# Kernel tuning notes

Hardware: AMD Instinct MI355X
Metric: run time of the kernel (lower is better)

Reference implementation:

```python
import jax, jax.numpy as jnp
import numpy as np
from jax import lax

B, T, D = 8, 2048, 1024
DECAY = 0.99
EPS = 1e-5


def _layer_norm(x, w, b):
    mu = jnp.mean(x, axis=-1, keepdims=True)
    var = jnp.var(x, axis=-1, keepdims=True)
    return (x - mu) * lax.rsqrt(var + EPS) * w + b


def _fixed_decay_scan(v, decay):
    # h_t = decay * h_{t-1} + v_t along axis=1, h_0 = v_0 (zero initial state)
    a = jnp.full_like(v, decay)

    def combine(c1, c2):
        a1, b1 = c1
        a2, b2 = c2
        return (a1 * a2, a2 * b1 + b2)

    _, h = lax.associative_scan(combine, (a, v), axis=1)
    return h


def setup_inputs() -> dict:
    key = jax.random.key(0)
    ks = jax.random.split(key, 12)
    s = 0.02
    return {
        "x": jax.random.normal(ks[0], (B, T, D), dtype=jnp.float32),
        "mask": jnp.ones((B, T), dtype=jnp.float32),
        "ln1_w": jnp.ones((D,), jnp.float32),
        "ln1_b": jnp.zeros((D,), jnp.float32),
        "ln2_w": jnp.ones((D,), jnp.float32),
        "ln2_b": jnp.zeros((D,), jnp.float32),
        "Wg_f": jax.random.normal(ks[1], (D, D), jnp.float32) * s,
        "bg_f": jnp.ones((D,), jnp.float32),
        "Wg_b": jax.random.normal(ks[2], (D, D), jnp.float32) * s,
        "bg_b": jnp.ones((D,), jnp.float32),
        "W_fuse": jax.random.normal(ks[3], (2 * D, D), jnp.float32) * s,
        "b_fuse": jnp.zeros((D,), jnp.float32),
        "W_ffn1": jax.random.normal(ks[4], (D, 2 * D), jnp.float32) * s,
        "b_ffn1": jnp.zeros((2 * D,), jnp.float32),
        "W_ffn2": jax.random.normal(ks[5], (2 * D, D), jnp.float32) * s,
        "b_ffn2": jnp.zeros((D,), jnp.float32),
    }


def reference(x, mask, ln1_w, ln1_b, ln2_w, ln2_b, Wg_f, bg_f, Wg_b, bg_b,
              W_fuse, b_fuse, W_ffn1, b_ffn1, W_ffn2, b_ffn2):
    residual = x
    h = _layer_norm(x, ln1_w, ln1_b)
    m = mask[..., None]  # (B,T,1)

    # forward-direction gated scan
    v_fwd = jax.nn.sigmoid(h @ Wg_f + bg_f) * h * m
    h_fwd = _fixed_decay_scan(v_fwd, DECAY)

    # backward-direction gated scan (scan over reversed time)
    v_bwd = jax.nn.sigmoid(h @ Wg_b + bg_b) * h * m
    h_bwd = jnp.flip(_fixed_decay_scan(jnp.flip(v_bwd, axis=1), DECAY), axis=1)

    # learned fusion gate
    beta = jax.nn.sigmoid(jnp.concatenate([h_fwd, h_bwd], axis=-1) @ W_fuse + b_fuse)
    fused = beta * h_fwd + (1.0 - beta) * h_bwd

    x = residual + fused  # dropout is identity in eval mode

    # FFN block (exact GELU as torch nn.GELU default)
    ffn = jax.nn.gelu(_layer_norm(x, ln2_w, ln2_b) @ W_ffn1 + b_ffn1, approximate=False) @ W_ffn2 + b_ffn2
    return x + ffn
```

## Files before the change

kernel.cpp:

```cpp
#include <hip/hip_runtime.h>
#include <math.h>

#define Bq 8
#define Tq 2048
#define Dq 1024
#define Mq (Bq*Tq)
#define NCHq 32
#define CHUNKq 64
#define DECAYq 0.99f
#define DF64q 0.52559646f
#define SGq (Bq*NCHq*4)
#define CEBNDq ((size_t)Bq*NCHq*Dq)

typedef unsigned short u16;
typedef unsigned int u32;
typedef __attribute__((ext_vector_type(8))) short bf16x8;
typedef __attribute__((ext_vector_type(4))) float f32x4;
typedef __attribute__((ext_vector_type(4))) u16 u16x4;

__device__ __forceinline__ u16 f2bf(float f) {
  u32 u = __builtin_bit_cast(u32, f);
  return (u16)((u + 0x7FFFu + ((u >> 16) & 1u)) >> 16);
}
__device__ __forceinline__ float bf2f(u16 h) {
  return __builtin_bit_cast(float, (u32)h << 16);
}
__device__ __forceinline__ float sigm(float x) { return 1.0f / (1.0f + expf(-x)); }

__global__ __launch_bounds__(256)
void transpose_all(const float* __restrict__ s0, u16* __restrict__ d0,
                   const float* __restrict__ s1, u16* __restrict__ d1,
                   const float* __restrict__ s2, u16* __restrict__ d2,
                   const float* __restrict__ s3, u16* __restrict__ d3,
                   const float* __restrict__ s4, u16* __restrict__ d4) {
  const int bid = blockIdx.x;
  const float* src; u16* dst; int K, N, local;
  if (bid < 1024)      { src = s0; dst = d0; K = 1024; N = 1024; local = bid; }
  else if (bid < 2048) { src = s1; dst = d1; K = 1024; N = 1024; local = bid - 1024; }
  else if (bid < 4096) { src = s2; dst = d2; K = 2048; N = 1024; local = bid - 2048; }
  else if (bid < 6144) { src = s3; dst = d3; K = 1024; N = 2048; local = bid - 4096; }
  else                 { src = s4; dst = d4; K = 2048; N = 1024; local = bid - 6144; }
  const int ntx = N >> 5;
  const int n0 = (local % ntx) << 5;
  const int k0 = (local / ntx) << 5;
  __shared__ float tile[32][33];
  const int tx = threadIdx.x & 31;
  const int ty = threadIdx.x >> 5;
#pragma unroll
  for (int j = 0; j < 32; j += 8)
    tile[ty + j][tx] = src[(size_t)(k0 + ty + j) * N + (n0 + tx)];
  __syncthreads();
#pragma unroll
  for (int j = 0; j < 32; j += 8)
    dst[(size_t)(n0 + ty + j) * K + (k0 + tx)] = f2bf(tile[tx][ty + j]);
}

__global__ __launch_bounds__(256)
void ln_kernel(const float* __restrict__ xin, const float* __restrict__ w,
               const float* __restrict__ bb, u16* __restrict__ obf) {
  const int row = blockIdx.x;
  const int tid = threadIdx.x;
  const float4 v = ((const float4*)(xin + (size_t)row * Dq))[tid];
  float s  = v.x + v.y + v.z + v.w;
  float s2 = v.x*v.x + v.y*v.y + v.z*v.z + v.w*v.w;
#pragma unroll
  for (int o = 32; o > 0; o >>= 1) { s += __shfl_xor(s, o); s2 += __shfl_xor(s2, o); }
  __shared__ float rs[4], rq[4];
  const int wid = tid >> 6;
  if ((tid & 63) == 0) { rs[wid] = s; rq[wid] = s2; }
  __syncthreads();
  s  = rs[0] + rs[1] + rs[2] + rs[3];
  s2 = rq[0] + rq[1] + rq[2] + rq[3];
  const float mu  = s * (1.0f/Dq);
  const float var = s2 * (1.0f/Dq) - mu*mu;
  const float inv = rsqrtf(var + 1e-5f);
  const float4 wv = ((const float4*)w)[tid];
  const float4 bv = ((const float4*)bb)[tid];
  float4 o;
  o.x = (v.x - mu)*inv*wv.x + bv.x;
  o.y = (v.y - mu)*inv*wv.y + bv.y;
  o.z = (v.z - mu)*inv*wv.z + bv.z;
  o.w = (v.w - mu)*inv*wv.w + bv.w;
  u16x4 ob; ob[0] = f2bf(o.x); ob[1] = f2bf(o.y); ob[2] = f2bf(o.z); ob[3] = f2bf(o.w);
  ((u16x4*)(obf + (size_t)row * Dq))[tid] = ob;
}

__global__ __launch_bounds__(256)
void scan_pass1_dual(const u16* __restrict__ vf, const u16* __restrict__ vb,
                     float* __restrict__ ce) {
  int bid = blockIdx.x;
  const bool rev = bid >= SGq;
  if (rev) bid -= SGq;
  const int dblk = bid & 3;
  const int c    = (bid >> 2) & 31;
  const int b    = bid >> 7;
  const int d    = (dblk << 8) + threadIdx.x;
  const u16* v   = rev ? vb : vf;
  float* cep     = ce + (rev ? CEBNDq : 0);
  const long step = rev ? -(long)Dq : (long)Dq;
  size_t idx = ((size_t)b * Tq + (rev ? (Tq - 1 - c * CHUNKq) : c * CHUNKq)) * Dq + d;
  float e = 0.0f;
  for (int i = 0; i < CHUNKq; ++i) { e = DECAYq * e + bf2f(v[idx]); idx += step; }
  cep[((size_t)b * NCHq + c) * Dq + d] = e;
}

__global__ __launch_bounds__(256)
void scan_pass2_dual(const float* __restrict__ ce, float* __restrict__ car) {
  const int idx = blockIdx.x * 256 + threadIdx.x;
  const int dir = idx >> 13;
  const int loc = idx & 8191;
  const int b = loc >> 10;
  const int d = loc & 1023;
  const size_t base = (size_t)dir * CEBNDq;
  float c = 0.0f;
  for (int k = 0; k < NCHq; ++k) {
    const size_t i = base + ((size_t)b * NCHq + k) * Dq + d;
    car[i] = c;
    c = DF64q * c + ce[i];
  }
}

__global__ __launch_bounds__(256)
void scan_pass3_dual(u16* __restrict__ vf, u16* __restrict__ vb,
                     const float* __restrict__ car) {
  int bid = blockIdx.x;
  const bool rev = bid >= SGq;
  if (rev) bid -= SGq;
  const int dblk = bid & 3;
  const int c    = (bid >> 2) & 31;
  const int b    = bid >> 7;
  const int d    = (dblk << 8) + threadIdx.x;
  u16* v = rev ? vb : vf;
  const float* carp = car + (rev ? CEBNDq : 0);
  float hc = carp[((size_t)b * NCHq + c) * Dq + d];
  const long step = rev ? -(long)Dq : (long)Dq;
  size_t idx = ((size_t)b * Tq + (rev ? (Tq - 1 - c * CHUNKq) : c * CHUNKq)) * Dq + d;
  for (int i = 0; i < CHUNKq; ++i) {
    hc = DECAYq * hc + bf2f(v[idx]);
    v[idx] = f2bf(hc);
    idx += step;
  }
}

struct EpiGate {
  const u16* h; const float* mask; const float* bgf; const float* bgb;
  u16* vf; u16* vb;
  __device__ void operator()(int r, int c, float val) const {
    const bool fwd = c < 1024;
    const int cc = c & 1023;
    const float s = sigm(val + (fwd ? bgf[cc] : bgb[cc]));
    const float hv = bf2f(h[(size_t)r * Dq + cc]) * mask[r];
    (fwd ? vf : vb)[(size_t)r * Dq + cc] = f2bf(s * hv);
  }
};
struct EpiFuse {
  const float* bfuse; const float* x; const u16* hf; const u16* hb; float* x2;
  __device__ void operator()(int r, int c, float val) const {
    const size_t i = (size_t)r * Dq + c;
    const float bta = sigm(val + bfuse[c]);
    x2[i] = x[i] + bta * bf2f(hf[i]) + (1.0f - bta) * bf2f(hb[i]);
  }
};
struct EpiFfn1 {
  const float* b1; u16* a;
  __device__ void operator()(int r, int c, float val) const {
    const float u = val + b1[c];
    const float g = 0.5f * u * (1.0f + erff(u * 0.70710678118f));
    a[(size_t)r * 2048 + c] = f2bf(g);
  }
};
struct EpiFfn2 {
  const float* b2; const float* x2; float* o;
  __device__ void operator()(int r, int c, float val) const {
    const size_t i = (size_t)r * Dq + c;
    o[i] = val + b2[c] + x2[i];
  }
};

template<typename Epi>
__global__ __launch_bounds__(512)
void gemm_bt(const u16* __restrict__ A, const u16* __restrict__ A2, int ksplit,
             const u16* __restrict__ BT, int K, int nx, Epi epi) {
  __shared__ u16 As[2][8192];
  __shared__ u16 Bs[2][8192];
  const int tid  = threadIdx.x;
  const int lane = tid & 63;
  const int w    = tid >> 6;
  const int wr   = w >> 2;
  const int wc   = w & 3;

  const int lin = blockIdx.x;
  const int q8  = gridDim.x >> 3;
  const int t   = (lin & 7) * q8 + (lin >> 3);
  const int by  = t / nx;
  const int bx  = t - by * nx;
  const int rowBase = by << 7;
  const int colBase = bx << 7;

  const int srow  = tid >> 3;
  const int scolE = (((tid & 7) ^ (srow & 7)) << 4) >> 1;
  const int KA    = (ksplit < K) ? ksplit : K;

  auto stage = [&](int buf, int kt) {
    const int kbase = kt << 6;
    const u16* Abase = (kbase < ksplit) ? A : A2;
    const int  kA    = (kbase < ksplit) ? kbase : (kbase - ksplit);
#pragma unroll
    for (int qq = 0; qq < 2; ++qq) {
      const u16* ga = Abase + (size_t)(rowBase + (qq << 6) + srow) * KA + kA + scolE;
      const u16* gb = BT    + (size_t)(colBase + (qq << 6) + srow) * K + kbase + scolE;
      __builtin_amdgcn_global_load_lds(
          (const __attribute__((address_space(1))) void*)ga,
          (__attribute__((address_space(3))) void*)(&As[buf][0] + (qq << 12) + (w << 9)), 16, 0, 0);
      __builtin_amdgcn_global_load_lds(
          (const __attribute__((address_space(1))) void*)gb,
          (__attribute__((address_space(3))) void*)(&Bs[buf][0] + (qq << 12) + (w << 9)), 16, 0, 0);
    }
  };

  f32x4 acc[4][2];
#pragma unroll
  for (int m = 0; m < 4; ++m)
#pragma unroll
    for (int n = 0; n < 2; ++n) acc[m][n] = (f32x4){0.f, 0.f, 0.f, 0.f};

  const int nkt = K >> 6;
  stage(0, 0);
  asm volatile("s_waitcnt vmcnt(0)" ::: "memory");
  __builtin_amdgcn_s_barrier();

  int cur = 0;
  for (int kt = 0; kt < nkt; ++kt) {
    if (kt + 1 < nkt) stage(cur ^ 1, kt + 1);
    const char* Ab = (const char*)&As[cur][0];
    const char* Bb = (const char*)&Bs[cur][0];
#pragma unroll
    for (int kk = 0; kk < 2; ++kk) {
      bf16x8 af[4], bfr[2];
      const int cb = (kk << 6) + ((lane >> 4) << 4);
#pragma unroll
      for (int m = 0; m < 4; ++m) {
        const int r = (wr << 6) + (m << 4) + (lane & 15);
        af[m] = *(const bf16x8*)(Ab + (r << 7) + (cb ^ ((r & 7) << 4)));
      }
#pragma unroll
      for (int n = 0; n < 2; ++n) {
        const int r = (wc << 5) + (n << 4) + (lane & 15);
        bfr[n] = *(const bf16x8*)(Bb + (r << 7) + (cb ^ ((r & 7) << 4)));
      }
#pragma unroll
      for (int m = 0; m < 4; ++m)
#pragma unroll
        for (int n = 0; n < 2; ++n)
          acc[m][n] = __builtin_amdgcn_mfma_f32_16x16x32_bf16(af[m], bfr[n], acc[m][n], 0, 0, 0);
    }
    __builtin_amdgcn_sched_barrier(0);
    asm volatile("s_waitcnt vmcnt(0) lgkmcnt(0)" ::: "memory");
    __builtin_amdgcn_s_barrier();
    cur ^= 1;
  }

#pragma unroll
  for (int m = 0; m < 4; ++m) {
    const int grow0 = rowBase + (wr << 6) + (m << 4) + ((lane >> 4) << 2);
#pragma unroll
    for (int n = 0; n < 2; ++n) {
      const int gcol = colBase + (wc << 5) + (n << 4) + (lane & 15);
#pragma unroll
      for (int r2 = 0; r2 < 4; ++r2)
        epi(grow0 + r2, gcol, acc[m][n][r2]);
    }
  }
}

extern "C" void kernel_launch(void* const* d_in, const int* in_sizes, int n_in,
                              void* d_out, int out_size, void* d_ws, size_t ws_size,
                              hipStream_t stream) {
  (void)in_sizes; (void)n_in; (void)out_size; (void)ws_size;
  const float* x      = (const float*)d_in[0];
  const float* mask   = (const float*)d_in[1];
  const float* ln1w   = (const float*)d_in[2];
  const float* ln1b   = (const float*)d_in[3];
  const float* ln2w   = (const float*)d_in[4];
  const float* ln2b   = (const float*)d_in[5];
  const float* Wg_f   = (const float*)d_in[6];
  const float* bg_f   = (const float*)d_in[7];
  const float* Wg_b   = (const float*)d_in[8];
  const float* bg_b   = (const float*)d_in[9];
  const float* W_fuse = (const float*)d_in[10];
  const float* b_fuse = (const float*)d_in[11];
  const float* W_ffn1 = (const float*)d_in[12];
  const float* b_ffn1 = (const float*)d_in[13];
  const float* W_ffn2 = (const float*)d_in[14];
  const float* b_ffn2 = (const float*)d_in[15];
  float* out = (float*)d_out;

  char* ws = (char*)d_ws;
  size_t off = 0;
  auto alloc = [&](size_t bytes) { char* p = ws + off; off += (bytes + 255) & ~(size_t)255; return p; };
  float* x2     = (float*)alloc((size_t)Mq * Dq * 4);
  u16*   slotA  = (u16*)  alloc((size_t)Mq * Dq * 2);
  u16*   hf_bf  = (u16*)  alloc((size_t)Mq * Dq * 2);
  u16*   hb_bf  = (u16*)  alloc((size_t)Mq * Dq * 2);
  u16*   WgT    = (u16*)  alloc((size_t)2048 * 1024 * 2);
  u16*   WfuT   = (u16*)  alloc((size_t)1024 * 2048 * 2);
  u16*   Wf1T   = (u16*)  alloc((size_t)2048 * 1024 * 2);
  u16*   Wf2T   = (u16*)  alloc((size_t)1024 * 2048 * 2);
  float* ce     = (float*)alloc(2 * CEBNDq * 4);
  float* car    = (float*)alloc(2 * CEBNDq * 4);
  u16*   h_bf16 = slotA;
  u16*   y2     = slotA;
  u16*   a_bf16 = hf_bf;

  transpose_all<<<8192, 256, 0, stream>>>(Wg_f, WgT, Wg_b, WgT + 1024 * 1024,
                                          W_fuse, WfuT, W_ffn1, Wf1T, W_ffn2, Wf2T);

  ln_kernel<<<Mq, 256, 0, stream>>>(x, ln1w, ln1b, h_bf16);

  EpiGate eg{h_bf16, mask, bg_f, bg_b, hf_bf, hb_bf};
  gemm_bt<EpiGate><<<16 * (Mq / 128), 512, 0, stream>>>(h_bf16, h_bf16, 1024, WgT, 1024, 16, eg);

  scan_pass1_dual<<<2 * SGq, 256, 0, stream>>>(hf_bf, hb_bf, ce);
  scan_pass2_dual<<<64, 256, 0, stream>>>(ce, car);
  scan_pass3_dual<<<2 * SGq, 256, 0, stream>>>(hf_bf, hb_bf, car);

  EpiFuse ef{b_fuse, x, hf_bf, hb_bf, x2};
  gemm_bt<EpiFuse><<<8 * (Mq / 128), 512, 0, stream>>>(hf_bf, hb_bf, 1024, WfuT, 2048, 8, ef);

  ln_kernel<<<Mq, 256, 0, stream>>>(x2, ln2w, ln2b, y2);

  EpiFfn1 e1{b_ffn1, a_bf16};
  gemm_bt<EpiFfn1><<<16 * (Mq / 128), 512, 0, stream>>>(y2, y2, 1024, Wf1T, 1024, 16, e1);

  EpiFfn2 e2{b_ffn2, x2, out};
  gemm_bt<EpiFfn2><<<8 * (Mq / 128), 512, 0, stream>>>(a_bf16, a_bf16, 2048, Wf2T, 2048, 8, e2);
}
```

Measured before the change: 515.3 us.

## Enlarge GEMM tiles to 256x256 with staggered A/B prefetch pipeline

Raises the GEMM block tile from 128x128 to 256x256, so each wave accumulates 128x64 outputs (32 MFMA accumulators). Global-to-LDS loads are split into halves and interleaved with the MFMA sub-steps, with A prefetched one K-step ahead and B two steps ahead, and barriers are placed around each sub-step. MFMA issue priority is raised with s_setprio. The aim is more data reuse per LDS byte and better overlap of memory traffic with compute. In exchange it adds heavy register pressure (128 accumulator floats per thread), launches 4x fewer blocks (256-512 blocks) which may under-fill 256 CUs, and adds more barriers.

```diff
diff --git a/kernel.cpp b/kernel.cpp
--- a/kernel.cpp
+++ b/kernel.cpp
@@ -181,8 +181,8 @@
 __global__ __launch_bounds__(512)
 void gemm_bt(const u16* __restrict__ A, const u16* __restrict__ A2, int ksplit,
              const u16* __restrict__ BT, int K, int nx, Epi epi) {
-  __shared__ u16 As[2][8192];
-  __shared__ u16 Bs[2][8192];
+  __shared__ u16 As[2][2][128][64];
+  __shared__ u16 Bs[2][2][128][64];
   const int tid  = threadIdx.x;
   const int lane = tid & 63;
   const int w    = tid >> 6;
@@ -194,78 +194,108 @@
   const int t   = (lin & 7) * q8 + (lin >> 3);
   const int by  = t / nx;
   const int bx  = t - by * nx;
-  const int rowBase = by << 7;
-  const int colBase = bx << 7;
+  const int rowBase = by << 8;
+  const int colBase = bx << 8;
 
   const int srow  = tid >> 3;
   const int scolE = (((tid & 7) ^ (srow & 7)) << 4) >> 1;
   const int KA    = (ksplit < K) ? ksplit : K;
 
-  auto stage = [&](int buf, int kt) {
+  auto stageA = [&](int buf, int kt, int half) {
     const int kbase = kt << 6;
-    const u16* Abase = (kbase < ksplit) ? A : A2;
-    const int  kA    = (kbase < ksplit) ? kbase : (kbase - ksplit);
-#pragma unroll
-    for (int qq = 0; qq < 2; ++qq) {
-      const u16* ga = Abase + (size_t)(rowBase + (qq << 6) + srow) * KA + kA + scolE;
-      const u16* gb = BT    + (size_t)(colBase + (qq << 6) + srow) * K + kbase + scolE;
+    const u16* Ab = (kbase < ksplit) ? A : A2;
+    const int  kA = (kbase < ksplit) ? kbase : (kbase - ksplit);
+#pragma unroll
+    for (int q = 0; q < 2; ++q) {
+      const u16* ga = Ab + (size_t)(rowBase + (half << 7) + (q << 6) + srow) * KA + kA + scolE;
       __builtin_amdgcn_global_load_lds(
           (const __attribute__((address_space(1))) void*)ga,
-          (__attribute__((address_space(3))) void*)(&As[buf][0] + (qq << 12) + (w << 9)), 16, 0, 0);
+          (__attribute__((address_space(3))) void*)((char*)&As[buf][half][0][0] + (q << 13) + (tid << 4)),
+          16, 0, 0);
+    }
+  };
+  auto stageB = [&](int buf, int kt, int half) {
+    const int kbase = kt << 6;
+#pragma unroll
+    for (int q = 0; q < 2; ++q) {
+      const u16* gb = BT + (size_t)(colBase + (half << 7) + (q << 6) + srow) * K + kbase + scolE;
       __builtin_amdgcn_global_load_lds(
           (const __attribute__((address_space(1))) void*)gb,
-          (__attribute__((address_space(3))) void*)(&Bs[buf][0] + (qq << 12) + (w << 9)), 16, 0, 0);
+          (__attribute__((address_space(3))) void*)((char*)&Bs[buf][half][0][0] + (q << 13) + (tid << 4)),
+          16, 0, 0);
     }
   };
 
-  f32x4 acc[4][2];
-#pragma unroll
-  for (int m = 0; m < 4; ++m)
-#pragma unroll
-    for (int n = 0; n < 2; ++n) acc[m][n] = (f32x4){0.f, 0.f, 0.f, 0.f};
+  f32x4 acc[8][4];
+#pragma unroll
+  for (int m = 0; m < 8; ++m)
+#pragma unroll
+    for (int n = 0; n < 4; ++n) acc[m][n] = (f32x4){0.f, 0.f, 0.f, 0.f};
 
   const int nkt = K >> 6;
-  stage(0, 0);
-  asm volatile("s_waitcnt vmcnt(0)" ::: "memory");
-  __builtin_amdgcn_s_barrier();
-
-  int cur = 0;
+  stageA(0, 0, 0); stageA(0, 0, 1);
+  stageB(0, 0, 0); stageB(0, 0, 1);
+  stageB(1, 1, 0); stageB(1, 1, 1);
+  asm volatile("s_waitcnt vmcnt(4)" ::: "memory");
+  asm volatile("s_barrier" ::: "memory");
+
   for (int kt = 0; kt < nkt; ++kt) {
-    if (kt + 1 < nkt) stage(cur ^ 1, kt + 1);
-    const char* Ab = (const char*)&As[cur][0];
-    const char* Bb = (const char*)&Bs[cur][0];
-#pragma unroll
-    for (int kk = 0; kk < 2; ++kk) {
-      bf16x8 af[4], bfr[2];
-      const int cb = (kk << 6) + ((lane >> 4) << 4);
-#pragma unroll
-      for (int m = 0; m < 4; ++m) {
-        const int r = (wr << 6) + (m << 4) + (lane & 15);
-        af[m] = *(const bf16x8*)(Ab + (r << 7) + (cb ^ ((r & 7) << 4)));
+    const int  cbuf = kt & 1;
+    const bool sA = (kt + 1) < nkt;
+    const bool sB = (kt + 2) < nkt;
+    const char* AsW = (const char*)&As[cbuf][wr][0][0];
+    const char* BsW = (const char*)&Bs[cbuf][wc >> 1][0][0];
+    bf16x8 bfr[2][4];
+#pragma unroll
+    for (int p = 0; p < 4; ++p) {
+      bf16x8 af[2][2];
+#pragma unroll
+      for (int i = 0; i < 2; ++i)
+#pragma unroll
+        for (int kk = 0; kk < 2; ++kk) {
+          const int r  = (p << 5) + (i << 4) + (lane & 15);
+          const int cb = (kk << 6) + ((lane >> 4) << 4);
+          af[i][kk] = *(const bf16x8*)(AsW + (r << 7) + (cb ^ ((r & 7) << 4)));
+        }
+      if (p == 0) {
+#pragma unroll
+        for (int kk = 0; kk < 2; ++kk)
+#pragma unroll
+          for (int n = 0; n < 4; ++n) {
+            const int r  = ((wc & 1) << 6) + (n << 4) + (lane & 15);
+            const int cb = (kk << 6) + ((lane >> 4) << 4);
+            bfr[kk][n] = *(const bf16x8*)(BsW + (r << 7) + (cb ^ ((r & 7) << 4)));
+          }
       }
-#pragma unroll
-      for (int n = 0; n < 2; ++n) {
-        const int r = (wc << 5) + (n << 4) + (lane & 15);
-        bfr[n] = *(const bf16x8*)(Bb + (r << 7) + (cb ^ ((r & 7) << 4)));
+      if (p == 0 && sA) stageA(cbuf ^ 1, kt + 1, 0);
+      if (p == 1 && sA) stageA(cbuf ^ 1, kt + 1, 1);
+      if (p == 2 && sB) stageB(cbuf, kt + 2, 0);
+      if (p == 3 && sB) stageB(cbuf, kt + 2, 1);
+      asm volatile("s_barrier" ::: "memory");
+      __builtin_amdgcn_s_setprio(1);
+#pragma unroll
+      for (int kk = 0; kk < 2; ++kk)
+#pragma unroll
+        for (int i = 0; i < 2; ++i)
+#pragma unroll
+          for (int n = 0; n < 4; ++n)
+            acc[(p << 1) + i][n] = __builtin_amdgcn_mfma_f32_16x16x32_bf16(
+                af[i][kk], bfr[kk][n], acc[(p << 1) + i][n], 0, 0, 0);
+      __builtin_amdgcn_s_setprio(0);
+      if (p == 3) {
+        if (sB)      asm volatile("s_waitcnt vmcnt(4)" ::: "memory");
+        else if (sA) asm volatile("s_waitcnt vmcnt(0)" ::: "memory");
       }
-#pragma unroll
-      for (int m = 0; m < 4; ++m)
-#pragma unroll
-        for (int n = 0; n < 2; ++n)
-          acc[m][n] = __builtin_amdgcn_mfma_f32_16x16x32_bf16(af[m], bfr[n], acc[m][n], 0, 0, 0);
+      asm volatile("s_barrier" ::: "memory");
     }
-    __builtin_amdgcn_sched_barrier(0);
-    asm volatile("s_waitcnt vmcnt(0) lgkmcnt(0)" ::: "memory");
-    __builtin_amdgcn_s_barrier();
-    cur ^= 1;
-  }
-
-#pragma unroll
-  for (int m = 0; m < 4; ++m) {
-    const int grow0 = rowBase + (wr << 6) + (m << 4) + ((lane >> 4) << 2);
-#pragma unroll
-    for (int n = 0; n < 2; ++n) {
-      const int gcol = colBase + (wc << 5) + (n << 4) + (lane & 15);
+  }
+
+#pragma unroll
+  for (int m = 0; m < 8; ++m) {
+    const int grow0 = rowBase + (wr << 7) + (m << 4) + ((lane >> 4) << 2);
+#pragma unroll
+    for (int n = 0; n < 4; ++n) {
+      const int gcol = colBase + (wc << 6) + (n << 4) + (lane & 15);
 #pragma unroll
       for (int r2 = 0; r2 < 4; ++r2)
         epi(grow0 + r2, gcol, acc[m][n][r2]);
@@ -318,20 +348,20 @@
   ln_kernel<<<Mq, 256, 0, stream>>>(x, ln1w, ln1b, h_bf16);
 
   EpiGate eg{h_bf16, mask, bg_f, bg_b, hf_bf, hb_bf};
-  gemm_bt<EpiGate><<<16 * (Mq / 128), 512, 0, stream>>>(h_bf16, h_bf16, 1024, WgT, 1024, 16, eg);
+  gemm_bt<EpiGate><<<8 * (Mq / 256), 512, 0, stream>>>(h_bf16, h_bf16, 1024, WgT, 1024, 8, eg);
 
   scan_pass1_dual<<<2 * SGq, 256, 0, stream>>>(hf_bf, hb_bf, ce);
   scan_pass2_dual<<<64, 256, 0, stream>>>(ce, car);
   scan_pass3_dual<<<2 * SGq, 256, 0, stream>>>(hf_bf, hb_bf, car);
 
   EpiFuse ef{b_fuse, x, hf_bf, hb_bf, x2};
-  gemm_bt<EpiFuse><<<8 * (Mq / 128), 512, 0, stream>>>(hf_bf, hb_bf, 1024, WfuT, 2048, 8, ef);
+  gemm_bt<EpiFuse><<<4 * (Mq / 256), 512, 0, stream>>>(hf_bf, hb_bf, 1024, WfuT, 2048, 4, ef);
 
   ln_kernel<<<Mq, 256, 0, stream>>>(x2, ln2w, ln2b, y2);
 
   EpiFfn1 e1{b_ffn1, a_bf16};
-  gemm_bt<EpiFfn1><<<16 * (Mq / 128), 512, 0, stream>>>(y2, y2, 1024, Wf1T, 1024, 16, e1);
+  gemm_bt<EpiFfn1><<<8 * (Mq / 256), 512, 0, stream>>>(y2, y2, 1024, Wf1T, 1024, 8, e1);
 
   EpiFfn2 e2{b_ffn2, x2, out};
-  gemm_bt<EpiFfn2><<<8 * (Mq / 128), 512, 0, stream>>>(a_bf16, a_bf16, 2048, Wf2T, 2048, 8, e2);
-}
+  gemm_bt<EpiFfn2><<<4 * (Mq / 256), 512, 0, stream>>>(a_bf16, a_bf16, 2048, Wf2T, 2048, 4, e2);
+}
```

After: 687.6 us. 1.33x slower.
